# Kernel tuning notes

Hardware: AMD Instinct MI355X
Metric: run time of the kernel (lower is better)

Reference implementation:

```python
import jax, jax.numpy as jnp
import numpy as np

N_NODES = 50000
N_EDGES = 1000000
IN_CH = 128
OUT_CH = 128
N_HEADS = 8
CIS = 8.0


def _edge_conv(x, e, wq, bq, wk, bk, wv, bv, n_heads, cis):
    """One EdgeConv layer (PyG mean aggregation, source_to_target flow)."""
    src, dst = e[0], e[1]                       # x_j = x[src], x_i = x[dst]
    xi = x[dst]
    xj = x[src]
    feat = jnp.concatenate([xi, xj - xi], axis=1)        # [E, 2C]
    q = feat @ wq + bq                                   # [E, O]
    k = feat @ wk + bk
    v = feat @ wv + bv
    E, O = q.shape
    hs = O // n_heads
    q = q.reshape(E, n_heads, hs)
    k = k.reshape(E, n_heads, hs)
    v = v.reshape(E, n_heads, hs)
    # edge_weight = sign(log|dst-src| - log(cis))
    d = jnp.abs(dst - src).astype(q.dtype)
    ew = jnp.sign(jnp.log(d) - jnp.log(jnp.asarray(cis, q.dtype)))
    v = v * ew[:, None, None]
    scale = jnp.asarray(1.0 / np.sqrt(hs), q.dtype)
    probs = jax.nn.softmax(q * k * scale, axis=-1)       # softmax over head_size
    ctx = (probs * v).reshape(E, O)                      # [E, O]
    n = x.shape[0]
    s = jax.ops.segment_sum(ctx, dst, num_segments=n)    # mean aggr over targets
    cnt = jax.ops.segment_sum(jnp.ones((E,), ctx.dtype), dst, num_segments=n)
    return s / jnp.maximum(cnt, 1.0)[:, None]


def setup_inputs() -> dict:
    key = jax.random.key(0)
    ks = jax.random.split(key, 24)
    x = jax.random.normal(ks[0], (N_NODES, IN_CH), jnp.float32)
    edge_index = jax.random.randint(ks[1], (2, N_EDGES), 0, N_NODES, dtype=jnp.int32)
    half = N_EDGES // 2
    e0 = edge_index[:, jax.random.permutation(ks[2], N_EDGES)[:half]]
    e1 = edge_index[:, jax.random.permutation(ks[3], N_EDGES)[:half]]
    e2 = edge_index[:, jax.random.permutation(ks[4], N_EDGES)[:half]]
    batch = jnp.zeros((N_NODES,), jnp.int32)

    def mk(k, i, o):
        return jax.random.normal(k, (i, o), jnp.float32) * 0.02

    def mkb(k, o):
        return jax.random.normal(k, (o,), jnp.float32) * 0.02

    # layer dims: conv0 128->128, conv1 128->64, conv2 64->128
    return dict(
        x=x, e0=e0, e1=e1, e2=e2, batch=batch,
        wq0=mk(ks[5], 2 * IN_CH, OUT_CH), bq0=mkb(ks[6], OUT_CH),
        wk0=mk(ks[7], 2 * IN_CH, OUT_CH), bk0=mkb(ks[8], OUT_CH),
        wv0=mk(ks[9], 2 * IN_CH, OUT_CH), bv0=mkb(ks[10], OUT_CH),
        wq1=mk(ks[11], 2 * OUT_CH, OUT_CH // 2), bq1=mkb(ks[12], OUT_CH // 2),
        wk1=mk(ks[13], 2 * OUT_CH, OUT_CH // 2), bk1=mkb(ks[14], OUT_CH // 2),
        wv1=mk(ks[15], 2 * OUT_CH, OUT_CH // 2), bv1=mkb(ks[16], OUT_CH // 2),
        wq2=mk(ks[17], OUT_CH, OUT_CH), bq2=mkb(ks[18], OUT_CH),
        wk2=mk(ks[19], OUT_CH, OUT_CH), bk2=mkb(ks[20], OUT_CH),
        wv2=mk(ks[21], OUT_CH, OUT_CH), bv2=mkb(ks[22], OUT_CH),
    )


def reference(x, e0, e1, e2, batch,
              wq0, bq0, wk0, bk0, wv0, bv0,
              wq1, bq1, wk1, bk1, wv1, bv1,
              wq2, bq2, wk2, bk2, wv2, bv2):
    x0 = jax.nn.relu(_edge_conv(x, e0, wq0, bq0, wk0, bk0, wv0, bv0, N_HEADS, CIS))
    h = jax.nn.relu(_edge_conv(x0, e1, wq1, bq1, wk1, bk1, wv1, bv1, N_HEADS, CIS))
    h = _edge_conv(h, e2, wq2, bq2, wk2, bk2, wv2, bv2, N_HEADS, CIS)
    return jax.nn.relu(h + x0)
```

## Files before the change

### kernel.cpp

```cpp
#include <hip/hip_runtime.h>


typedef short bf16x8 __attribute__((ext_vector_type(8)));
typedef unsigned int u32x4 __attribute__((ext_vector_type(4)));
typedef float f32x4 __attribute__((ext_vector_type(4)));
typedef float f32x2 __attribute__((ext_vector_type(2)));

__device__ __forceinline__ unsigned short f2bf(float f) {
  unsigned int u = __float_as_uint(f);
  u += 0x7FFFu + ((u >> 16) & 1u);
  return (unsigned short)(u >> 16);
}
__device__ __forceinline__ float b2f(short s) {
  return __uint_as_float(((unsigned)(unsigned short)s) << 16);
}
__device__ __forceinline__ f32x2 bfpair(unsigned w) {
  f32x2 r;
  r.x = __uint_as_float(w << 16);
  r.y = __uint_as_float(w & 0xffff0000u);
  return r;
}

__device__ __forceinline__ void pack_w_seg(const float* __restrict__ wq,
                                           const float* __restrict__ wk,
                                           const float* __restrict__ wv,
                                           unsigned short* __restrict__ dst,
                                           int IN, int O, float kscale, int id) {
  int kchunks = IN >> 5, nchunks = O >> 4;
  int total = 6 * nchunks * kchunks * 64;
  if (id >= total) return;
  int lane = id & 63;
  int frag = id >> 6;
  int kc = frag % kchunks;
  int nc = (frag / kchunks) % nchunks;
  int mat = frag / (kchunks * nchunks);
  const float* w = (mat % 3 == 0) ? wq : (mat % 3 == 1) ? wk : wv;
  float mul = (mat % 3 == 1) ? kscale : 1.0f;
  int n = nc * 16 + (lane & 15);
  int k0 = kc * 32 + (lane >> 4) * 8;
  unsigned short tmp[8];
#pragma unroll
  for (int j = 0; j < 8; ++j) {
    int row = k0 + j;
    float bot = w[(size_t)(IN + row) * O + n];
    float val = (mat < 3) ? (w[(size_t)row * O + n] - bot) : bot;
    tmp[j] = f2bf(val * mul);
  }
  uint4 o;
  o.x = (unsigned)tmp[0] | ((unsigned)tmp[1] << 16);
  o.y = (unsigned)tmp[2] | ((unsigned)tmp[3] << 16);
  o.z = (unsigned)tmp[4] | ((unsigned)tmp[5] << 16);
  o.w = (unsigned)tmp[6] | ((unsigned)tmp[7] << 16);
  reinterpret_cast<uint4*>(dst)[id] = o;
}

__device__ __forceinline__ void pack_b_seg(const float* __restrict__ bq,
                                           const float* __restrict__ bk,
                                           const float* __restrict__ bv, float kscale, int O,
                                           float* __restrict__ out, int i) {
  int mat = i / O, c = i % O;
  float v = 0.f;
  if (mat == 0) v = bq[c];
  else if (mat == 1) v = bk[c] * kscale;
  else if (mat == 2) v = bv[c];
  out[i] = v;
}

__global__ void preproc(
    uint4* __restrict__ z0, int n0, uint4* __restrict__ z1, int n1,
    uint4* __restrict__ z2, int n2,
    const float* __restrict__ x, unsigned short* __restrict__ xb, int n8,
    const float* __restrict__ wq0, const float* __restrict__ wk0, const float* __restrict__ wv0,
    const float* __restrict__ wq1, const float* __restrict__ wk1, const float* __restrict__ wv1,
    const float* __restrict__ wq2, const float* __restrict__ wk2, const float* __restrict__ wv2,
    unsigned short* __restrict__ wp0, unsigned short* __restrict__ wp1,
    unsigned short* __restrict__ wp2,
    const float* __restrict__ bq0, const float* __restrict__ bk0, const float* __restrict__ bv0,
    const float* __restrict__ bq1, const float* __restrict__ bk1, const float* __restrict__ bv1,
    const float* __restrict__ bq2, const float* __restrict__ bk2, const float* __restrict__ bv2,
    float* __restrict__ bias0, float* __restrict__ bias1, float* __restrict__ bias2,
    float sc16, float sc8) {
  const int tid = blockIdx.x * blockDim.x + threadIdx.x;
  const int stride = gridDim.x * blockDim.x;
  const uint4 Z = make_uint4(0u, 0u, 0u, 0u);
  for (int j = tid; j < n0; j += stride) z0[j] = Z;
  for (int j = tid; j < n1; j += stride) z1[j] = Z;
  for (int j = tid; j < n2; j += stride) z2[j] = Z;
  for (int j = tid; j < n8; j += stride) {
    float4 a = reinterpret_cast<const float4*>(x)[2 * j];
    float4 b = reinterpret_cast<const float4*>(x)[2 * j + 1];
    uint4 o;
    o.x = (unsigned)f2bf(a.x) | ((unsigned)f2bf(a.y) << 16);
    o.y = (unsigned)f2bf(a.z) | ((unsigned)f2bf(a.w) << 16);
    o.z = (unsigned)f2bf(b.x) | ((unsigned)f2bf(b.y) << 16);
    o.w = (unsigned)f2bf(b.z) | ((unsigned)f2bf(b.w) << 16);
    reinterpret_cast<uint4*>(xb)[j] = o;
  }
  if (tid < 12288) pack_w_seg(wq0, wk0, wv0, wp0, 128, 128, sc16, tid);
  else if (tid < 18432) pack_w_seg(wq1, wk1, wv1, wp1, 128, 64, sc8, tid - 12288);
  else if (tid < 24576) pack_w_seg(wq2, wk2, wv2, wp2, 64, 128, sc16, tid - 18432);
  else if (tid < 24576 + 1920) {
    int i = tid - 24576;
    if (i < 768) pack_b_seg(bq0, bk0, bv0, sc16, 128, bias0, i);
    else if (i < 1152) pack_b_seg(bq1, bk1, bv1, sc8, 64, bias1, i - 768);
    else pack_b_seg(bq2, bk2, bv2, sc16, 128, bias2, i - 1152);
  }
}

__global__ void hist3(const int* __restrict__ e0, const int* __restrict__ e1,
                      const int* __restrict__ e2, int E, int* __restrict__ hist,
                      int* __restrict__ rank, int NP) {
  int i = blockIdx.x * blockDim.x + threadIdx.x;
  if (i >= E) return;
  rank[0 * E + i] = atomicAdd(&hist[0 * NP + e0[E + i]], 1);
  rank[1 * E + i] = atomicAdd(&hist[1 * NP + e1[E + i]], 1);
  rank[2 * E + i] = atomicAdd(&hist[2 * NP + e2[E + i]], 1);
}

__device__ __forceinline__ int block_scan_excl256(int v, int* buf, int t, int* total) {
  buf[t] = v;
  __syncthreads();
#pragma unroll
  for (int off = 1; off < 256; off <<= 1) {
    int add = (t >= off) ? buf[t - off] : 0;
    __syncthreads();
    buf[t] += add;
    __syncthreads();
  }
  int incl = buf[t];
  *total = buf[255];
  __syncthreads();
  return incl - v;
}

__global__ void scan_pass1(const int* __restrict__ hist, int* __restrict__ excl,
                           int* __restrict__ bsum, int n, int NP) {
  __shared__ int buf[256];
  int y = blockIdx.y, t = threadIdx.x;
  int i = blockIdx.x * 256 + t;
  int v = (i < n) ? hist[y * NP + i] : 0;
  int total;
  int ex = block_scan_excl256(v, buf, t, &total);
  if (i < NP) excl[y * NP + i] = ex;
  if (t == 0) bsum[y * 256 + blockIdx.x] = total;
}

__global__ void scan_pass2(int* __restrict__ bsum, int nblk) {
  __shared__ int buf[256];
  int y = blockIdx.y, t = threadIdx.x;
  int v = (t < nblk) ? bsum[y * 256 + t] : 0;
  int total;
  int ex = block_scan_excl256(v, buf, t, &total);
  bsum[y * 256 + t] = ex;
}

__global__ void scan_pass3(const int* __restrict__ excl, const int* __restrict__ bsum,
                           int* __restrict__ rowptr, int n, int NP, int RP, int E) {
  int y = blockIdx.y;
  int i = blockIdx.x * 256 + threadIdx.x;
  if (i < n) rowptr[y * RP + i] = excl[y * NP + i] + bsum[y * 256 + blockIdx.x];
  if (i == 0) rowptr[y * RP + n] = E;
}

__global__ void scatter3(const int* __restrict__ e0, const int* __restrict__ e1,
                         const int* __restrict__ e2, int E, const int* __restrict__ rowptr,
                         const int* __restrict__ rank, long long* __restrict__ pairs,
                         int NP, int RP) {
  int y = blockIdx.y;
  const int* e = (y == 0) ? e0 : (y == 1) ? e1 : e2;
  int i = blockIdx.x * 256 + threadIdx.x;
  if (i >= E) return;
  int sN = e[i], d = e[E + i];
  int pos = rowptr[y * RP + d] + rank[(size_t)y * E + i];
  long long val = ((long long)(unsigned)d << 32) | (unsigned)sN;
  __builtin_nontemporal_store(val, &pairs[(size_t)y * E + pos]);
}

template <int IN, int O, int G>
__global__ __launch_bounds__(256, 4) void node_gemm(
    const unsigned short* __restrict__ xb, int N, int NT,
    const unsigned short* __restrict__ wpack, const float* __restrict__ bias6,
    unsigned short* __restrict__ Y1, unsigned short* __restrict__ Y2) {
  constexpr int KC = IN / 32;
  constexpr int NCH = O / 16;
  constexpr int CHR = IN / 8;
  constexpr int CM = CHR - 1;
  __shared__ unsigned short tiles[64 * IN];

  const int chunk = gridDim.x >> 3;
  const int lb = (blockIdx.x & 7) * chunk + (blockIdx.x >> 3);
  if (lb >= NT * G) return;
  const int tile = lb / G;
  const int grp = lb % G;

  const int t = threadIdx.x, w = t >> 6, ln = t & 63;
  const int n0 = tile * 64;

  {
    constexpr int RPI = 64 / CHR;
    constexpr int NI = 16 / RPI;
    const int r_in = ln / CHR, c = ln % CHR;
#pragma unroll
    for (int i = 0; i < NI; ++i) {
      int row = w * 16 + i * RPI + r_in;
      int node = min(n0 + row, N - 1);
      int sc = c ^ (row & CM);
      const unsigned short* g = xb + (size_t)node * IN + sc * 8;
      unsigned short* l = &tiles[(size_t)(w * 16 + i * RPI) * IN];
      __builtin_amdgcn_global_load_lds(
          (const __attribute__((address_space(1))) unsigned int*)g,
          (__attribute__((address_space(3))) unsigned int*)l, 16, 0, 0);
    }
  }
  __syncthreads();

  const int col = ln & 15, quad = ln >> 4;
  const int g0 = grp * 8 + w * 2;

  f32x4 acc[2][4];
#pragma unroll
  for (int cc = 0; cc < 2; ++cc)
#pragma unroll
    for (int m = 0; m < 4; ++m) acc[cc][m] = (f32x4){0.f, 0.f, 0.f, 0.f};

#pragma unroll
  for (int kc = 0; kc < KC; ++kc) {
    bf16x8 a[4];
#pragma unroll
    for (int m = 0; m < 4; ++m) {
      int row = m * 16 + col;
      int sc = (kc * 4 + quad) ^ (row & CM);
      a[m] = *reinterpret_cast<const bf16x8*>(&tiles[(size_t)row * IN + sc * 8]);
    }
#pragma unroll
    for (int cc = 0; cc < 2; ++cc) {
      const bf16x8 b = *reinterpret_cast<const bf16x8*>(
          wpack + ((size_t)((g0 + cc) * KC + kc) * 64 + ln) * 8);
#pragma unroll
      for (int m = 0; m < 4; ++m)
        acc[cc][m] = __builtin_amdgcn_mfma_f32_16x16x32_bf16(a[m], b, acc[cc][m], 0, 0, 0);
    }
  }

#pragma unroll
  for (int cc = 0; cc < 2; ++cc) {
    int gch = g0 + cc;
    int mat = gch / NCH, ncg = gch % NCH;
    unsigned short* Yp = (mat < 3) ? Y1 : Y2;
    int mo = (mat < 3) ? mat : mat - 3;
    float bv = bias6[gch * 16 + col];
    size_t coloff = (size_t)mo * O + ncg * 16 + col;
#pragma unroll
    for (int m = 0; m < 4; ++m)
#pragma unroll
      for (int r = 0; r < 4; ++r) {
        int node = n0 + m * 16 + quad * 4 + r;
        if (node < N) Yp[(size_t)node * (3 * O) + coloff] = f2bf(acc[cc][m][r] + bv);
      }
  }
}

template <int O, int HS>
__global__ __launch_bounds__(512, 6) void edge_attn_kernel(
    const unsigned short* __restrict__ Y1, const unsigned short* __restrict__ Y2,
    const int2* __restrict__ pairs, const int E, float* __restrict__ s) {
  constexpr int NL = HS / 8;
  constexpr int PM = O / 4 - 1;
  __shared__ float ctx[64 * O];
  __shared__ int dstL[64];

  const int chunkB = gridDim.x >> 3;
  const int lb = (blockIdx.x & 7) * chunkB + (blockIdx.x >> 3);
  if (lb * 64 >= E) return;

  const int t = threadIdx.x;
  const int e = t >> 3, head = t & 7;
  const int eG = lb * 64 + e;
  const int eC = min(eG, E - 1);
  const bool valid = eG < E;
  const int2 p = pairs[eC];
  const int sN = p.x, dN = p.y;
  if ((t & 7) == 0) dstL[e] = dN;
  const float dd = fabsf((float)(dN - sN));
  const float ew = (dd > 8.f) ? 1.f : ((dd == 8.f) ? 0.f : -1.f);

  const unsigned short* b1 = Y1 + (size_t)dN * (3 * O) + head * HS;
  const unsigned short* b2 = Y2 + (size_t)sN * (3 * O) + head * HS;

  u32x4 q1[NL], q2[NL], k1[NL], k2[NL], v1[NL], v2[NL];
#pragma unroll
  for (int l = 0; l < NL; ++l) {
    q1[l] = *reinterpret_cast<const u32x4*>(b1 + l * 8);
    q2[l] = *reinterpret_cast<const u32x4*>(b2 + l * 8);
    k1[l] = *reinterpret_cast<const u32x4*>(b1 + O + l * 8);
    k2[l] = *reinterpret_cast<const u32x4*>(b2 + O + l * 8);
    v1[l] = *reinterpret_cast<const u32x4*>(b1 + 2 * O + l * 8);
    v2[l] = *reinterpret_cast<const u32x4*>(b2 + 2 * O + l * 8);
  }

  f32x2 ex2[NL * 4];
  f32x2 sum2 = (f32x2){0.f, 0.f};
#pragma unroll
  for (int l = 0; l < NL; ++l)
#pragma unroll
    for (int d = 0; d < 4; ++d) {
      f32x2 q = bfpair(q1[l][d]) + bfpair(q2[l][d]);
      f32x2 k = bfpair(k1[l][d]) + bfpair(k2[l][d]);
      f32x2 qk = q * k;
      f32x2 eo;
      eo.x = exp2f(qk.x);
      eo.y = exp2f(qk.y);
      ex2[l * 4 + d] = eo;
      sum2 += eo;
    }
  const float sum = sum2.x + sum2.y;
  const float rs = valid ? (ew / sum) : 0.f;
  const f32x2 rs2 = (f32x2){rs, rs};
#pragma unroll
  for (int l = 0; l < NL; ++l) {
#pragma unroll
    for (int g2 = 0; g2 < 2; ++g2) {
      f32x2 oa = ex2[l * 4 + g2 * 2] * rs2 * (bfpair(v1[l][g2 * 2]) + bfpair(v2[l][g2 * 2]));
      f32x2 ob = ex2[l * 4 + g2 * 2 + 1] * rs2 *
                 (bfpair(v1[l][g2 * 2 + 1]) + bfpair(v2[l][g2 * 2 + 1]));
      f32x4 o = (f32x4){oa.x, oa.y, ob.x, ob.y};
      int g = l * 2 + g2;
      int pch = (g * 8 + head + e) & PM;
      *reinterpret_cast<f32x4*>(&ctx[e * O + pch * 4]) = o;
    }
  }
  __syncthreads();

  {
    constexpr int GRP = 512 / O;
    constexpr int EPT = 64 / GRP;
    const int hs2 = t & 7;
    const int cs = (t >> 3) & (HS - 1);
    const int colA = hs2 * HS + cs;
    const int seg0 = (t / O) * EPT;
    const int inv = (cs >> 2) * 8 + hs2;
    const int js = cs & 3;
    float run = 0.f;
    int runstart = 0;
    int dcur = dstL[seg0];
#pragma unroll
    for (int i = 0; i < EPT; ++i) {
      int ee = seg0 + i;
      int pch = (inv + ee) & PM;
      run += ctx[ee * O + pch * 4 + js];
      int dnext = (i < EPT - 1) ? dstL[ee + 1] : -1;
      if (dnext != dcur) {
        float* addr = &s[(size_t)dcur * O + colA];
        if (runstart > 0 && i < EPT - 1) *addr = run;
        else atomicAdd(addr, run);
        run = 0.f;
        runstart = i + 1;
        dcur = dnext;
      }
    }
  }
}

__global__ void finalize_relu_f32bf16(float* __restrict__ s, const int* __restrict__ rowptr,
                                      unsigned short* __restrict__ xbo, int total4, int Odiv4) {
  int i = blockIdx.x * blockDim.x + threadIdx.x;
  if (i >= total4) return;
  int node = i / Odiv4;
  float c = fmaxf((float)(rowptr[node + 1] - rowptr[node]), 1.0f);
  float4 v = reinterpret_cast<float4*>(s)[i];
  v.x = fmaxf(v.x / c, 0.f);
  v.y = fmaxf(v.y / c, 0.f);
  v.z = fmaxf(v.z / c, 0.f);
  v.w = fmaxf(v.w / c, 0.f);
  reinterpret_cast<float4*>(s)[i] = v;
  ushort4 o = make_ushort4(f2bf(v.x), f2bf(v.y), f2bf(v.z), f2bf(v.w));
  reinterpret_cast<ushort4*>(xbo)[i] = o;
}

__global__ void finalize_relu_bf16(const float* __restrict__ s, const int* __restrict__ rowptr,
                                   unsigned short* __restrict__ xbo, int total4, int Odiv4) {
  int i = blockIdx.x * blockDim.x + threadIdx.x;
  if (i >= total4) return;
  int node = i / Odiv4;
  float c = fmaxf((float)(rowptr[node + 1] - rowptr[node]), 1.0f);
  float4 v = reinterpret_cast<const float4*>(s)[i];
  ushort4 o = make_ushort4(f2bf(fmaxf(v.x / c, 0.f)), f2bf(fmaxf(v.y / c, 0.f)),
                           f2bf(fmaxf(v.z / c, 0.f)), f2bf(fmaxf(v.w / c, 0.f)));
  reinterpret_cast<ushort4*>(xbo)[i] = o;
}

__global__ void finalize_add_relu(float* __restrict__ out, const float* __restrict__ x0,
                                  const int* __restrict__ rowptr, int total4, int Odiv4) {
  int i = blockIdx.x * blockDim.x + threadIdx.x;
  if (i >= total4) return;
  int node = i / Odiv4;
  float c = fmaxf((float)(rowptr[node + 1] - rowptr[node]), 1.0f);
  float4 v = reinterpret_cast<float4*>(out)[i];
  float4 r = reinterpret_cast<const float4*>(x0)[i];
  v.x = fmaxf(v.x / c + r.x, 0.f);
  v.y = fmaxf(v.y / c + r.y, 0.f);
  v.z = fmaxf(v.z / c + r.z, 0.f);
  v.w = fmaxf(v.w / c + r.w, 0.f);
  reinterpret_cast<float4*>(out)[i] = v;
}

extern "C" void kernel_launch(void* const* d_in, const int* in_sizes, int n_in,
                              void* d_out, int out_size, void* d_ws, size_t ws_size,
                              hipStream_t stream) {
  const float* x = (const float*)d_in[0];
  const int* e0 = (const int*)d_in[1];
  const int* e1 = (const int*)d_in[2];
  const int* e2 = (const int*)d_in[3];
  const float* wq0 = (const float*)d_in[5];
  const float* bq0 = (const float*)d_in[6];
  const float* wk0 = (const float*)d_in[7];
  const float* bk0 = (const float*)d_in[8];
  const float* wv0 = (const float*)d_in[9];
  const float* bv0 = (const float*)d_in[10];
  const float* wq1 = (const float*)d_in[11];
  const float* bq1 = (const float*)d_in[12];
  const float* wk1 = (const float*)d_in[13];
  const float* bk1 = (const float*)d_in[14];
  const float* wv1 = (const float*)d_in[15];
  const float* bv1 = (const float*)d_in[16];
  const float* wq2 = (const float*)d_in[17];
  const float* bq2 = (const float*)d_in[18];
  const float* wk2 = (const float*)d_in[19];
  const float* bk2 = (const float*)d_in[20];
  const float* wv2 = (const float*)d_in[21];
  const float* bv2 = (const float*)d_in[22];

  const int N = in_sizes[0] / 128;
  const int E = in_sizes[1] / 2;
  const int NBLK = (N + 255) / 256;
  const int NP = NBLK * 256;
  const int RP = NP + 256;
  const float LOG2E = 1.4426950408889634f;
  const float SC16 = 0.25f * LOG2E;
  const float SC8 = 0.35355339059327373f * LOG2E;

  unsigned short* wp0 = (unsigned short*)d_ws;
  unsigned short* wp1 = wp0 + 98304;
  unsigned short* wp2 = wp1 + 49152;
  float* bias0 = (float*)(wp2 + 49152);
  float* bias1 = bias0 + 768;
  float* bias2 = bias1 + 384;
  unsigned short* xb = (unsigned short*)(bias2 + 768);
  unsigned short* Y1 = xb + (size_t)N * 128;
  unsigned short* Y2 = Y1 + (size_t)N * 384;
  float* s0 = (float*)(Y2 + (size_t)N * 384);
  float* s1 = s0 + (size_t)N * 128;
  int* hist = (int*)(s1 + (size_t)N * 64);
  int* excl = hist + 3 * (size_t)NP;
  int* bsum = excl + 3 * (size_t)NP;
  int* rowptr = bsum + 768;
  int* rank = rowptr + 3 * (size_t)RP;
  long long* pairs = (long long*)(rank + 3 * (size_t)E + 2);

  preproc<<<2048, 256, 0, stream>>>(
      (uint4*)hist, 3 * NP / 4, (uint4*)s0, N * 48, (uint4*)d_out, out_size / 4,
      x, xb, N * 16,
      wq0, wk0, wv0, wq1, wk1, wv1, wq2, wk2, wv2, wp0, wp1, wp2,
      bq0, bk0, bv0, bq1, bk1, bv1, bq2, bk2, bv2, bias0, bias1, bias2,
      SC16, SC8);

  const int EB256 = (E + 255) / 256;
  hist3<<<EB256, 256, 0, stream>>>(e0, e1, e2, E, hist, rank, NP);
  scan_pass1<<<dim3(NBLK, 3), 256, 0, stream>>>(hist, excl, bsum, N, NP);
  scan_pass2<<<dim3(1, 3), 256, 0, stream>>>(bsum, NBLK);
  scan_pass3<<<dim3(NBLK, 3), 256, 0, stream>>>(excl, bsum, rowptr, N, NP, RP, E);
  scatter3<<<dim3(EB256, 3), 256, 0, stream>>>(e0, e1, e2, E, rowptr, rank, pairs, NP, RP);

  const int NT = (N + 63) / 64;
  const int EBK = (E + 63) / 64;
  const int EGRID = 8 * ((EBK + 7) / 8);
  const int GG6 = 8 * ((NT * 6 + 7) / 8);
  const int GG3 = 8 * ((NT * 3 + 7) / 8);

  node_gemm<128, 128, 6><<<GG6, 256, 0, stream>>>(xb, N, NT, wp0, bias0, Y1, Y2);
  edge_attn_kernel<128, 16><<<EGRID, 512, 0, stream>>>(Y1, Y2, (const int2*)pairs, E, s0);
  finalize_relu_f32bf16<<<(N * 32 + 255) / 256, 256, 0, stream>>>(s0, rowptr, xb, N * 32, 32);
  node_gemm<128, 64, 3><<<GG3, 256, 0, stream>>>(xb, N, NT, wp1, bias1, Y1, Y2);
  edge_attn_kernel<64, 8><<<EGRID, 512, 0, stream>>>(Y1, Y2, (const int2*)(pairs + E), E, s1);
  finalize_relu_bf16<<<(N * 16 + 255) / 256, 256, 0, stream>>>(s1, rowptr + RP, xb, N * 16, 16);
  node_gemm<64, 128, 6><<<GG6, 256, 0, stream>>>(xb, N, NT, wp2, bias2, Y1, Y2);
  edge_attn_kernel<128, 16><<<EGRID, 512, 0, stream>>>(Y1, Y2, (const int2*)(pairs + 2 * (size_t)E),
                                                       E, (float*)d_out);
  finalize_add_relu<<<(N * 32 + 255) / 256, 256, 0, stream>>>((float*)d_out, s0, rowptr + 2 * RP,
                                                              N * 32, 32);
}
```

Measured before the change: 531.7 us.

## Make edge attention kernel persistent with software-prefetched source rows

The edge attention kernel becomes a persistent kernel of 2048 blocks, each looping over its XCD's chunk of 64-edge groups with stride 256. The next group's pair and source-node Q/K/V rows are prefetched into registers while the current group is computed and reduced. The occupancy hint rises from 6 to 8 waves per SIMD. This is meant to hide gather latency and cut block launch overhead. The cost is extra register pressure from the prefetch buffers and an added barrier per iteration.

```diff
diff --git a/kernel.cpp b/kernel.cpp
--- a/kernel.cpp
+++ b/kernel.cpp
@@ -261,7 +261,7 @@
 }
 
 template <int O, int HS>
-__global__ __launch_bounds__(512, 6) void edge_attn_kernel(
+__global__ __launch_bounds__(512, 8) void edge_attn_kernel(
     const unsigned short* __restrict__ Y1, const unsigned short* __restrict__ Y2,
     const int2* __restrict__ pairs, const int E, float* __restrict__ s) {
   constexpr int NL = HS / 8;
@@ -269,95 +269,138 @@
   __shared__ float ctx[64 * O];
   __shared__ int dstL[64];
 
-  const int chunkB = gridDim.x >> 3;
-  const int lb = (blockIdx.x & 7) * chunkB + (blockIdx.x >> 3);
-  if (lb * 64 >= E) return;
-
+  const int NG = (E + 63) >> 6;
+  const int CPX = (NG + 7) >> 3;
+  const int xcd = blockIdx.x & 7;
+  const int j0 = blockIdx.x >> 3;
   const int t = threadIdx.x;
   const int e = t >> 3, head = t & 7;
-  const int eG = lb * 64 + e;
-  const int eC = min(eG, E - 1);
-  const bool valid = eG < E;
-  const int2 p = pairs[eC];
-  const int sN = p.x, dN = p.y;
-  if ((t & 7) == 0) dstL[e] = dN;
-  const float dd = fabsf((float)(dN - sN));
-  const float ew = (dd > 8.f) ? 1.f : ((dd == 8.f) ? 0.f : -1.f);
-
-  const unsigned short* b1 = Y1 + (size_t)dN * (3 * O) + head * HS;
-  const unsigned short* b2 = Y2 + (size_t)sN * (3 * O) + head * HS;
-
-  u32x4 q1[NL], q2[NL], k1[NL], k2[NL], v1[NL], v2[NL];
-#pragma unroll
-  for (int l = 0; l < NL; ++l) {
-    q1[l] = *reinterpret_cast<const u32x4*>(b1 + l * 8);
-    q2[l] = *reinterpret_cast<const u32x4*>(b2 + l * 8);
-    k1[l] = *reinterpret_cast<const u32x4*>(b1 + O + l * 8);
-    k2[l] = *reinterpret_cast<const u32x4*>(b2 + O + l * 8);
-    v1[l] = *reinterpret_cast<const u32x4*>(b1 + 2 * O + l * 8);
-    v2[l] = *reinterpret_cast<const u32x4*>(b2 + 2 * O + l * 8);
-  }
-
-  f32x2 ex2[NL * 4];
-  f32x2 sum2 = (f32x2){0.f, 0.f};
-#pragma unroll
-  for (int l = 0; l < NL; ++l)
-#pragma unroll
-    for (int d = 0; d < 4; ++d) {
-      f32x2 q = bfpair(q1[l][d]) + bfpair(q2[l][d]);
-      f32x2 k = bfpair(k1[l][d]) + bfpair(k2[l][d]);
-      f32x2 qk = q * k;
-      f32x2 eo;
-      eo.x = exp2f(qk.x);
-      eo.y = exp2f(qk.y);
-      ex2[l * 4 + d] = eo;
-      sum2 += eo;
-    }
-  const float sum = sum2.x + sum2.y;
-  const float rs = valid ? (ew / sum) : 0.f;
-  const f32x2 rs2 = (f32x2){rs, rs};
-#pragma unroll
-  for (int l = 0; l < NL; ++l) {
-#pragma unroll
-    for (int g2 = 0; g2 < 2; ++g2) {
-      f32x2 oa = ex2[l * 4 + g2 * 2] * rs2 * (bfpair(v1[l][g2 * 2]) + bfpair(v2[l][g2 * 2]));
-      f32x2 ob = ex2[l * 4 + g2 * 2 + 1] * rs2 *
-                 (bfpair(v1[l][g2 * 2 + 1]) + bfpair(v2[l][g2 * 2 + 1]));
-      f32x4 o = (f32x4){oa.x, oa.y, ob.x, ob.y};
-      int g = l * 2 + g2;
-      int pch = (g * 8 + head + e) & PM;
-      *reinterpret_cast<f32x4*>(&ctx[e * O + pch * 4]) = o;
-    }
-  }
-  __syncthreads();
-
+
+  int j = j0;
+  int lg = xcd * CPX + j;
+  if (j >= CPX || lg >= NG) return;
+
+  int eG = lg * 64 + e;
+  int2 p = pairs[min(eG, E - 1)];
+
+  u32x4 q2[NL], k2[NL], v2[NL];
   {
-    constexpr int GRP = 512 / O;
-    constexpr int EPT = 64 / GRP;
-    const int hs2 = t & 7;
-    const int cs = (t >> 3) & (HS - 1);
-    const int colA = hs2 * HS + cs;
-    const int seg0 = (t / O) * EPT;
-    const int inv = (cs >> 2) * 8 + hs2;
-    const int js = cs & 3;
-    float run = 0.f;
-    int runstart = 0;
-    int dcur = dstL[seg0];
-#pragma unroll
-    for (int i = 0; i < EPT; ++i) {
-      int ee = seg0 + i;
-      int pch = (inv + ee) & PM;
-      run += ctx[ee * O + pch * 4 + js];
-      int dnext = (i < EPT - 1) ? dstL[ee + 1] : -1;
-      if (dnext != dcur) {
-        float* addr = &s[(size_t)dcur * O + colA];
-        if (runstart > 0 && i < EPT - 1) *addr = run;
-        else atomicAdd(addr, run);
-        run = 0.f;
-        runstart = i + 1;
-        dcur = dnext;
+    const unsigned short* b2 = Y2 + (size_t)p.x * (3 * O) + head * HS;
+#pragma unroll
+    for (int l = 0; l < NL; ++l) {
+      q2[l] = *reinterpret_cast<const u32x4*>(b2 + l * 8);
+      k2[l] = *reinterpret_cast<const u32x4*>(b2 + O + l * 8);
+      v2[l] = *reinterpret_cast<const u32x4*>(b2 + 2 * O + l * 8);
+    }
+  }
+
+  while (true) {
+    const bool valid = eG < E;
+    const int sN = p.x, dN = p.y;
+    if ((t & 7) == 0) dstL[e] = dN;
+
+    const int jn = j + 256;
+    const int lgn = lg + 256;
+    const bool more = (jn < CPX) && (lgn < NG);
+    const int eGn = lgn * 64 + e;
+    int2 pN;
+    if (more) pN = pairs[min(eGn, E - 1)];
+
+    const float dd = fabsf((float)(dN - sN));
+    const float ew = (dd > 8.f) ? 1.f : ((dd == 8.f) ? 0.f : -1.f);
+
+    const unsigned short* b1 = Y1 + (size_t)dN * (3 * O) + head * HS;
+    u32x4 q1[NL], k1[NL];
+#pragma unroll
+    for (int l = 0; l < NL; ++l) {
+      q1[l] = *reinterpret_cast<const u32x4*>(b1 + l * 8);
+      k1[l] = *reinterpret_cast<const u32x4*>(b1 + O + l * 8);
+    }
+
+    f32x2 ex2[NL * 4];
+    f32x2 sum2 = (f32x2){0.f, 0.f};
+#pragma unroll
+    for (int l = 0; l < NL; ++l)
+#pragma unroll
+      for (int d = 0; d < 4; ++d) {
+        f32x2 q = bfpair(q1[l][d]) + bfpair(q2[l][d]);
+        f32x2 k = bfpair(k1[l][d]) + bfpair(k2[l][d]);
+        f32x2 qk = q * k;
+        f32x2 eo;
+        eo.x = exp2f(qk.x);
+        eo.y = exp2f(qk.y);
+        ex2[l * 4 + d] = eo;
+        sum2 += eo;
       }
-    }
+    const float sum = sum2.x + sum2.y;
+    const float rs = valid ? (ew / sum) : 0.f;
+    const f32x2 rs2 = (f32x2){rs, rs};
+
+    u32x4 v1[NL];
+#pragma unroll
+    for (int l = 0; l < NL; ++l)
+      v1[l] = *reinterpret_cast<const u32x4*>(b1 + 2 * O + l * 8);
+
+#pragma unroll
+    for (int l = 0; l < NL; ++l) {
+#pragma unroll
+      for (int g2 = 0; g2 < 2; ++g2) {
+        f32x2 oa = ex2[l * 4 + g2 * 2] * rs2 * (bfpair(v1[l][g2 * 2]) + bfpair(v2[l][g2 * 2]));
+        f32x2 ob = ex2[l * 4 + g2 * 2 + 1] * rs2 *
+                   (bfpair(v1[l][g2 * 2 + 1]) + bfpair(v2[l][g2 * 2 + 1]));
+        f32x4 o = (f32x4){oa.x, oa.y, ob.x, ob.y};
+        int g = l * 2 + g2;
+        int pch = (g * 8 + head + e) & PM;
+        *reinterpret_cast<f32x4*>(&ctx[e * O + pch * 4]) = o;
+      }
+    }
+
+    if (more) {
+      const unsigned short* b2 = Y2 + (size_t)pN.x * (3 * O) + head * HS;
+#pragma unroll
+      for (int l = 0; l < NL; ++l) {
+        q2[l] = *reinterpret_cast<const u32x4*>(b2 + l * 8);
+        k2[l] = *reinterpret_cast<const u32x4*>(b2 + O + l * 8);
+        v2[l] = *reinterpret_cast<const u32x4*>(b2 + 2 * O + l * 8);
+      }
+    }
+    __syncthreads();
+
+    {
+      constexpr int GRP = 512 / O;
+      constexpr int EPT = 64 / GRP;
+      const int hs2 = t & 7;
+      const int cs = (t >> 3) & (HS - 1);
+      const int colA = hs2 * HS + cs;
+      const int seg0 = (t / O) * EPT;
+      const int inv = (cs >> 2) * 8 + hs2;
+      const int js = cs & 3;
+      float run = 0.f;
+      int runstart = 0;
+      int dcur = dstL[seg0];
+#pragma unroll
+      for (int i = 0; i < EPT; ++i) {
+        int ee = seg0 + i;
+        int pch = (inv + ee) & PM;
+        run += ctx[ee * O + pch * 4 + js];
+        int dnext = (i < EPT - 1) ? dstL[ee + 1] : -1;
+        if (dnext != dcur) {
+          float* addr = &s[(size_t)dcur * O + colA];
+          if (runstart > 0 && i < EPT - 1) *addr = run;
+          else atomicAdd(addr, run);
+          run = 0.f;
+          runstart = i + 1;
+          dcur = dnext;
+        }
+      }
+    }
+
+    if (!more) break;
+    __syncthreads();
+    j = jn;
+    lg = lgn;
+    eG = eGn;
+    p = pN;
   }
 }
 
@@ -472,19 +515,18 @@
   scatter3<<<dim3(EB256, 3), 256, 0, stream>>>(e0, e1, e2, E, rowptr, rank, pairs, NP, RP);
 
   const int NT = (N + 63) / 64;
-  const int EBK = (E + 63) / 64;
-  const int EGRID = 8 * ((EBK + 7) / 8);
   const int GG6 = 8 * ((NT * 6 + 7) / 8);
   const int GG3 = 8 * ((NT * 3 + 7) / 8);
+  const int EPERS = 2048;
 
   node_gemm<128, 128, 6><<<GG6, 256, 0, stream>>>(xb, N, NT, wp0, bias0, Y1, Y2);
-  edge_attn_kernel<128, 16><<<EGRID, 512, 0, stream>>>(Y1, Y2, (const int2*)pairs, E, s0);
+  edge_attn_kernel<128, 16><<<EPERS, 512, 0, stream>>>(Y1, Y2, (const int2*)pairs, E, s0);
   finalize_relu_f32bf16<<<(N * 32 + 255) / 256, 256, 0, stream>>>(s0, rowptr, xb, N * 32, 32);
   node_gemm<128, 64, 3><<<GG3, 256, 0, stream>>>(xb, N, NT, wp1, bias1, Y1, Y2);
-  edge_attn_kernel<64, 8><<<EGRID, 512, 0, stream>>>(Y1, Y2, (const int2*)(pairs + E), E, s1);
+  edge_attn_kernel<64, 8><<<EPERS, 512, 0, stream>>>(Y1, Y2, (const int2*)(pairs + E), E, s1);
   finalize_relu_bf16<<<(N * 16 + 255) / 256, 256, 0, stream>>>(s1, rowptr + RP, xb, N * 16, 16);
   node_gemm<64, 128, 6><<<GG6, 256, 0, stream>>>(xb, N, NT, wp2, bias2, Y1, Y2);
-  edge_attn_kernel<128, 16><<<EGRID, 512, 0, stream>>>(Y1, Y2, (const int2*)(pairs + 2 * (size_t)E),
+  edge_attn_kernel<128, 16><<<EPERS, 512, 0, stream>>>(Y1, Y2, (const int2*)(pairs + 2 * (size_t)E),
                                                        E, (float*)d_out);
   finalize_add_relu<<<(N * 32 + 255) / 256, 256, 0, stream>>>((float*)d_out, s0, rowptr + 2 * RP,
                                                               N * 32, 32);
```

Measured after the change: 674.9 us. 26.9% more time.
